# Optimization experiments

Measured on AMD Instinct MI355X. Metric: run time of the kernel, lower is better.

## Reference

```python
import jax, jax.numpy as jnp
import numpy as np

# Faithful JAX port of predictTransform: YOLO anchor-box decode.
# prediction: [B, A*(5+C), G, G] raw conv output.
# Returns [B, G*G*A, 5+C] decoded boxes in input-image pixel units.

def setup_inputs() -> dict:
    key = jax.random.key(0)
    B, A, C, IN_DIM, G = 32, 3, 80, 608, 76  # stride = 608 // 76 = 8
    attrs = 5 + C
    prediction = jax.random.normal(key, (B, A * attrs, G, G), dtype=jnp.float32)
    # standard YOLOv3 anchors for the stride-8 head, in input-pixel units
    anchors = jnp.array([[10.0, 13.0], [16.0, 30.0], [33.0, 23.0]], dtype=jnp.float32)
    return {"prediction": prediction, "anchors": anchors, "inputDim": IN_DIM, "numClasses": C}


def reference(prediction, anchors, inputDim, numClasses):
    B = prediction.shape[0]
    stride = inputDim // prediction.shape[2]
    G = inputDim // stride
    A = anchors.shape[0]
    attrs = 5 + numClasses

    # [B, A*attrs, G*G] -> [B, G*G, A*attrs] -> [B, G*G*A, attrs]
    p = prediction.reshape(B, attrs * A, G * G)
    p = jnp.transpose(p, (0, 2, 1)).reshape(B, G * G * A, attrs)

    anc = anchors / stride  # anchors in grid units, [A, 2]

    # grid offsets: np.meshgrid(grid, grid) -> a[i,j]=j (x), b[i,j]=i (y)
    grid = jnp.arange(G, dtype=jnp.float32)
    gx, gy = jnp.meshgrid(grid, grid)  # each [G, G]
    xy = jnp.stack([gx.ravel(), gy.ravel()], axis=-1)        # [G*G, 2]
    xy = jnp.repeat(xy, A, axis=0)[None]                     # [1, G*G*A, 2]
    anc_t = jnp.tile(anc, (G * G, 1))[None]                  # [1, G*G*A, 2]

    txy = jax.nn.sigmoid(p[..., 0:2]) + xy                   # center x,y in grid units
    twh = jnp.exp(p[..., 2:4]) * anc_t                       # w,h in grid units
    conf = jax.nn.sigmoid(p[..., 4:5])                       # objectness
    cls = jax.nn.sigmoid(p[..., 5:])                         # class probs

    boxes = jnp.concatenate([txy, twh], axis=-1) * stride    # back to pixel units
    return jnp.concatenate([boxes, conf, cls], axis=-1)
```

## Files before the change

kernel.cpp:

```cpp
#include <hip/hip_runtime.h>


#define BATCH   32
#define ATTRS   85
#define CH      255
#define GRID    76
#define SP      5776
#define STRIDE_F 8.0f
#define S_TILE  64
#define TPB     1024
#define TILES_PER_B ((SP + S_TILE - 1) / S_TILE)
#define NF4_READ (CH * (S_TILE / 4))

typedef float f4 __attribute__((ext_vector_type(4)));

__global__ __launch_bounds__(TPB, 8) void yolo_decode_kernel(
        const float* __restrict__ pred,
        const float* __restrict__ anchors,
        float* __restrict__ out) {
    __shared__ float lds[S_TILE * CH];

    const int tid = threadIdx.x;
    const int bid = blockIdx.x;
    const int b   = bid / TILES_PER_B;
    const int t   = bid - b * TILES_PER_B;
    const int s0  = t * S_TILE;
    const int sw  = (SP - s0 < S_TILE) ? (SP - s0) : S_TILE;

    const float a0x = anchors[0], a0y = anchors[1];
    const float a1x = anchors[2], a1y = anchors[3];
    const float a2x = anchors[4], a2y = anchors[5];

    const float* __restrict__ src = pred + (size_t)b * (size_t)(CH * SP);
    for (int j = tid; j < NF4_READ; j += TPB) {
        const int c  = j >> 4;
        const int sl = (j & 15) * 4;
        if (sl >= sw) continue;

        f4 v = *(const f4*)(src + c * SP + s0 + sl);

        const int a    = c / ATTRS;
        const int attr = c - a * ATTRS;
        const float ax = (a == 0) ? a0x : (a == 1) ? a1x : a2x;
        const float ay = (a == 0) ? a0y : (a == 1) ? a1y : a2y;

        #pragma unroll
        for (int e = 0; e < 4; ++e) {
            const float val = v[e];
            const int   s   = s0 + sl + e;
            float r;
            if (attr == 2) {
                r = __expf(val) * ax;
            } else if (attr == 3) {
                r = __expf(val) * ay;
            } else {
                const float sg = __builtin_amdgcn_rcpf(1.0f + __expf(-val));
                if (attr == 0) {
                    const int x = s % GRID;
                    r = (sg + (float)x) * STRIDE_F;
                } else if (attr == 1) {
                    const int y = s / GRID;
                    r = (sg + (float)y) * STRIDE_F;
                } else {
                    r = sg;
                }
            }
            lds[(sl + e) * CH + c] = r;
        }
    }
    __syncthreads();

    const int nf4w = (sw * CH) >> 2;
    float* __restrict__ dst = out + (size_t)b * (size_t)(SP * CH) + (size_t)s0 * CH;
    for (int j = tid; j < nf4w; j += TPB) {
        f4 v = *(const f4*)(lds + j * 4);
        __builtin_nontemporal_store(v, (f4*)(dst + j * 4));
    }
}

extern "C" void kernel_launch(void* const* d_in, const int* in_sizes, int n_in,
                              void* d_out, int out_size, void* d_ws, size_t ws_size,
                              hipStream_t stream) {
    const float* pred    = (const float*)d_in[0];
    const float* anchors = (const float*)d_in[1];
    float* out = (float*)d_out;

    const int grid = BATCH * TILES_PER_B;
    yolo_decode_kernel<<<grid, TPB, 0, stream>>>(pred, anchors, out);
}
```

Baseline: 68.30 us.

## Use persistent blocks with double-buffered LDS and register prefetch of next tile

Replaces one-block-per-tile launch with 512 persistent blocks that loop over 32-position tiles. The next tile's input is loaded into registers before the current tile's transposed output is stored from a double-buffered LDS array. The intent is to overlap global reads with writes and cut block launch overhead, at the cost of smaller tiles and a fixed block count that may underfill the GPU or lower occupancy.

Result: slower. 76.05 us (+11.3%).

```diff
diff --git a/kernel.cpp b/kernel.cpp
--- a/kernel.cpp
+++ b/kernel.cpp
@@ -7,74 +7,102 @@
 #define GRID    76
 #define SP      5776
 #define STRIDE_F 8.0f
-#define S_TILE  64
+#define S_TILE  32
 #define TPB     1024
-#define TILES_PER_B ((SP + S_TILE - 1) / S_TILE)
-#define NF4_READ (CH * (S_TILE / 4))
+#define TILES_PER_B 181
+#define NTILES  (BATCH * TILES_PER_B)
+#define NBLK    512
+#define NF4     (CH * (S_TILE / 4))
 
 typedef float f4 __attribute__((ext_vector_type(4)));
+
+__device__ __forceinline__ float decode1(float val, int attr, int s,
+                                         float ax, float ay) {
+    if (attr == 2) return __expf(val) * ax;
+    if (attr == 3) return __expf(val) * ay;
+    const float sg = __builtin_amdgcn_rcpf(1.0f + __expf(-val));
+    if (attr == 0) return (sg + (float)(s % GRID)) * STRIDE_F;
+    if (attr == 1) return (sg + (float)(s / GRID)) * STRIDE_F;
+    return sg;
+}
 
 __global__ __launch_bounds__(TPB, 8) void yolo_decode_kernel(
         const float* __restrict__ pred,
         const float* __restrict__ anchors,
         float* __restrict__ out) {
-    __shared__ float lds[S_TILE * CH];
+    __shared__ float buf[2][S_TILE * CH];
 
     const int tid = threadIdx.x;
-    const int bid = blockIdx.x;
-    const int b   = bid / TILES_PER_B;
-    const int t   = bid - b * TILES_PER_B;
-    const int s0  = t * S_TILE;
-    const int sw  = (SP - s0 < S_TILE) ? (SP - s0) : S_TILE;
 
     const float a0x = anchors[0], a0y = anchors[1];
     const float a1x = anchors[2], a1y = anchors[3];
     const float a2x = anchors[4], a2y = anchors[5];
 
-    const float* __restrict__ src = pred + (size_t)b * (size_t)(CH * SP);
-    for (int j = tid; j < NF4_READ; j += TPB) {
-        const int c  = j >> 4;
-        const int sl = (j & 15) * 4;
-        if (sl >= sw) continue;
+    const int c0  = tid >> 3;
+    const int sl0 = (tid & 7) * 4;
+    const int j1  = tid + TPB;
+    const int c1  = j1 >> 3;
+    const int sl1 = (j1 & 7) * 4;
+    const bool have1 = (j1 < NF4);
 
-        f4 v = *(const f4*)(src + c * SP + s0 + sl);
+    const int aI0 = c0 / ATTRS, attr0 = c0 - aI0 * ATTRS;
+    const int aI1 = c1 / ATTRS, attr1 = c1 - aI1 * ATTRS;
+    const float ax0 = (aI0 == 0) ? a0x : (aI0 == 1) ? a1x : a2x;
+    const float ay0 = (aI0 == 0) ? a0y : (aI0 == 1) ? a1y : a2y;
+    const float ax1 = (aI1 == 0) ? a0x : (aI1 == 1) ? a1x : a2x;
+    const float ay1 = (aI1 == 0) ? a0y : (aI1 == 1) ? a1y : a2y;
 
-        const int a    = c / ATTRS;
-        const int attr = c - a * ATTRS;
-        const float ax = (a == 0) ? a0x : (a == 1) ? a1x : a2x;
-        const float ay = (a == 0) ? a0y : (a == 1) ? a1y : a2y;
+    int tk = blockIdx.x;
+    int b  = tk / TILES_PER_B;
+    int t  = tk - b * TILES_PER_B;
+    int s0 = t * S_TILE;
+    int sw = (t == TILES_PER_B - 1) ? (SP - s0) : S_TILE;
+    const float* src = pred + (size_t)b * ((size_t)CH * SP) + s0;
+
+    f4 v0 = {0.f, 0.f, 0.f, 0.f}, v1 = {0.f, 0.f, 0.f, 0.f};
+    if (sl0 < sw)          v0 = *(const f4*)(src + (size_t)c0 * SP + sl0);
+    if (have1 && sl1 < sw) v1 = *(const f4*)(src + (size_t)c1 * SP + sl1);
+
+    int it = 0;
+    for (;;) {
+        float* __restrict__ B = buf[it & 1];
+        const int cb = b, cs0 = s0, csw = sw;
 
         #pragma unroll
-        for (int e = 0; e < 4; ++e) {
-            const float val = v[e];
-            const int   s   = s0 + sl + e;
-            float r;
-            if (attr == 2) {
-                r = __expf(val) * ax;
-            } else if (attr == 3) {
-                r = __expf(val) * ay;
-            } else {
-                const float sg = __builtin_amdgcn_rcpf(1.0f + __expf(-val));
-                if (attr == 0) {
-                    const int x = s % GRID;
-                    r = (sg + (float)x) * STRIDE_F;
-                } else if (attr == 1) {
-                    const int y = s / GRID;
-                    r = (sg + (float)y) * STRIDE_F;
-                } else {
-                    r = sg;
-                }
-            }
-            lds[(sl + e) * CH + c] = r;
+        for (int e = 0; e < 4; ++e)
+            B[(sl0 + e) * CH + c0] = decode1(v0[e], attr0, cs0 + sl0 + e, ax0, ay0);
+        if (have1) {
+            #pragma unroll
+            for (int e = 0; e < 4; ++e)
+                B[(sl1 + e) * CH + c1] = decode1(v1[e], attr1, cs0 + sl1 + e, ax1, ay1);
         }
-    }
-    __syncthreads();
 
-    const int nf4w = (sw * CH) >> 2;
-    float* __restrict__ dst = out + (size_t)b * (size_t)(SP * CH) + (size_t)s0 * CH;
-    for (int j = tid; j < nf4w; j += TPB) {
-        f4 v = *(const f4*)(lds + j * 4);
-        __builtin_nontemporal_store(v, (f4*)(dst + j * 4));
+        const int ntk = tk + NBLK;
+        const bool more = (ntk < NTILES);
+        if (more) {
+            b  = ntk / TILES_PER_B;
+            t  = ntk - b * TILES_PER_B;
+            s0 = t * S_TILE;
+            sw = (t == TILES_PER_B - 1) ? (SP - s0) : S_TILE;
+            src = pred + (size_t)b * ((size_t)CH * SP) + s0;
+            if (sl0 < sw)          v0 = *(const f4*)(src + (size_t)c0 * SP + sl0);
+            if (have1 && sl1 < sw) v1 = *(const f4*)(src + (size_t)c1 * SP + sl1);
+        }
+
+        __syncthreads();
+
+        const float* __restrict__ Bs = buf[it & 1];
+        float* __restrict__ dst = out + (size_t)cb * ((size_t)SP * CH)
+                                      + (size_t)cs0 * CH;
+        const int nf4w = (csw * CH) >> 2;
+        for (int j = tid; j < nf4w; j += TPB) {
+            f4 w = *(const f4*)(Bs + j * 4);
+            __builtin_nontemporal_store(w, (f4*)(dst + j * 4));
+        }
+
+        if (!more) break;
+        tk = ntk;
+        ++it;
     }
 }
 
@@ -85,6 +113,5 @@
     const float* anchors = (const float*)d_in[1];
     float* out = (float*)d_out;
 
-    const int grid = BATCH * TILES_PER_B;
-    yolo_decode_kernel<<<grid, TPB, 0, stream>>>(pred, anchors, out);
+    yolo_decode_kernel<<<NBLK, TPB, 0, stream>>>(pred, anchors, out);
 }
```
